# Kernel tuning notes

Measured on AMD Instinct MI355X. Metric: run time of the kernel, lower is better.

## Reference

```python
import jax, jax.numpy as jnp
import numpy as np

jax.config.update("jax_enable_x64", True)

STRIDE = 1
PADDING = 1


def _im2col(x, k, s):
    # x: (n, c, H, W) already padded. Returns (n, c*k*k, oh*ow) with
    # channel-major, then (kh, kw) ordering -- matching torch unfold/img2col.
    n, c, H, W = x.shape
    oh = (H - k) // s + 1
    ow = (W - k) // s + 1
    # k*k = 9 slices: small fixed loop over kernel offsets, fully vectorized
    # over batch/channel/spatial dims.
    patches = jnp.stack(
        [x[:, :, i:i + s * (oh - 1) + 1:s, j:j + s * (ow - 1) + 1:s]
         for i in range(k) for j in range(k)],
        axis=2,
    )  # (n, c, k*k, oh, ow)
    return patches.reshape(n, c * k * k, oh * ow)


def setup_inputs() -> dict:
    key = jax.random.key(0)
    k1, k2, k3 = jax.random.split(key, 3)
    x = jax.random.randint(k1, (32, 64, 56, 56), 0, 65536, dtype=jnp.int64)
    weight = jax.random.randint(k2, (64, 64, 3, 3), 0, 65536, dtype=jnp.int64)
    bias = jax.random.randint(k3, (64,), 0, 65536, dtype=jnp.int64)
    return {"x": x, "weight": weight, "bias": bias}


def reference(x, weight, bias):
    kN, kC, k, _ = weight.shape
    n, c, H, W = x.shape
    oh = (H - k + 2 * PADDING) // STRIDE + 1
    ow = (W - k + 2 * PADDING) // STRIDE + 1
    # pad spatial dims with zeros (ring zero)
    xp = jnp.pad(x, ((0, 0), (0, 0), (PADDING, PADDING), (PADDING, PADDING)))
    cols = _im2col(xp, k, STRIDE)              # (n, c*k*k, L)
    cols_t = cols.transpose(0, 2, 1)           # (n, L, c*k*k)
    w2 = weight.reshape(kN, kC * k * k).T      # (c*k*k, kN)
    # int64 matmul: overflow wraps (two's complement), matching ring Z_{2^64}
    out = jnp.einsum('nlk,ko->nlo', cols_t, w2) + bias  # (n, L, kN)
    return out.transpose(0, 2, 1).reshape(n, kN, oh, ow)
```

## Files before the change

kernel.cpp:

```cpp
#include <hip/hip_runtime.h>


typedef int v4i __attribute__((ext_vector_type(4)));

#define LCOL 144
#define LROW (58 * LCOL)

__device__ __align__(16) unsigned char g_wb[2 * 9 * 64 * 64];
__device__ unsigned g_off[64];

static __device__ __forceinline__ unsigned bsum(unsigned v, unsigned acc) {
#if __has_builtin(__builtin_amdgcn_sad_u8)
    return __builtin_amdgcn_sad_u8(v, 0u, acc);
#else
    return acc + (v & 0xFFu) + ((v >> 8) & 0xFFu) + ((v >> 16) & 0xFFu) + (v >> 24);
#endif
}

__global__ __launch_bounds__(256) void packw(const int* __restrict__ w,
                                             const int* __restrict__ bias) {
    int blk = blockIdx.x;
    if (blk < 144) {
        int i = blk * 256 + threadIdx.x;
        if (i >= 64 * 64 * 9) return;
        int k = i / 576;
        int r = i - k * 576;
        int c = r / 9;
        int t = r - c * 9;
        unsigned v = (unsigned)w[i];
        g_wb[((0 * 9 + t) * 64 + k) * 64 + c] = (unsigned char)((v & 255u) ^ 0x80u);
        g_wb[((1 * 9 + t) * 64 + k) * 64 + c] = (unsigned char)(((v >> 8) & 255u) ^ 0x80u);
    } else {
        int k    = threadIdx.x >> 2;
        int part = threadIdx.x & 3;
        int s0 = 0, s1 = 0;
        for (int j = part * 144; j < part * 144 + 144; ++j) {
            unsigned W = (unsigned)w[k * 576 + j];
            s0 += (int)(W & 255u);
            s1 += (int)((W >> 8) & 255u);
        }
        s0 += __shfl_xor(s0, 1); s0 += __shfl_xor(s0, 2);
        s1 += __shfl_xor(s1, 1); s1 += __shfl_xor(s1, 2);
        if (part == 0) {
            s0 -= 73728;
            s1 -= 73728;
            unsigned ws = (unsigned)(s0 + 256 * s1);
            g_off[k] = (unsigned)bias[k] + 32896u * ws + 1082146816u * 576u;
        }
    }
}

__global__ __launch_bounds__(256, 2) void secconv(const int* __restrict__ x,
                                                  int* __restrict__ out)
{
    __shared__ unsigned char sx[6 * LROW];
    __shared__ int ss[6 * 58];

    const int tid  = threadIdx.x;
    const int blk  = blockIdx.x;
    const int q    = blk >> 3;
    const int rg   = q % 14;
    const int n    = (blk & 7) + 8 * (q / 14);
    const int wid  = tid >> 6;
    const int lane = tid & 63;
    const int lm   = lane & 15;
    const int lq   = lane >> 4;
    const int kp   = wid & 1;
    const int ph   = wid >> 1;
    const int kbase = kp * 32;

    for (int it = tid; it < 348; it += 256) {
        const int pr = it / 58, pc = it - pr * 58;
        const int ih = 4 * rg - 1 + pr, iw = pc - 1;
        unsigned char* ob = sx + pr * LROW + pc * LCOL;
        int S;
        if ((unsigned)ih < 56u && (unsigned)iw < 56u) {
            const int* xp = x + (long)n * 64 * 3136 + ih * 56 + iw;
            unsigned slo = 0, shi = 0;
#pragma unroll
            for (int g = 0; g < 4; ++g) {
                unsigned lo[4], hi[4];
#pragma unroll
                for (int u = 0; u < 4; ++u) {
                    const int c = g * 16 + u * 4;
                    unsigned v0 = (unsigned)xp[(c + 0) * 3136];
                    unsigned v1 = (unsigned)xp[(c + 1) * 3136];
                    unsigned v2 = (unsigned)xp[(c + 2) * 3136];
                    unsigned v3 = (unsigned)xp[(c + 3) * 3136];
                    unsigned t01 = __builtin_amdgcn_perm(v1, v0, 0x05040100u);
                    unsigned t23 = __builtin_amdgcn_perm(v3, v2, 0x05040100u);
                    unsigned lw  = __builtin_amdgcn_perm(t23, t01, 0x06040200u);
                    unsigned hw  = __builtin_amdgcn_perm(t23, t01, 0x07050301u);
                    slo = bsum(lw, slo);
                    shi = bsum(hw, shi);
                    lo[u] = lw ^ 0x80808080u;
                    hi[u] = hw ^ 0x80808080u;
                }
                *(uint4*)(ob + g * 16)      = make_uint4(lo[0], lo[1], lo[2], lo[3]);
                *(uint4*)(ob + 64 + g * 16) = make_uint4(hi[0], hi[1], hi[2], hi[3]);
            }
            S = (int)(slo + (shi << 8)) - 2105344;
        } else {
            uint4 v = make_uint4(0x80808080u, 0x80808080u, 0x80808080u, 0x80808080u);
#pragma unroll
            for (int g = 0; g < 4; ++g) {
                *(uint4*)(ob + g * 16)      = v;
                *(uint4*)(ob + 64 + g * 16) = v;
            }
            S = -2105344;
        }
        ss[it] = S;
    }

    v4i wf[2][2][9];
#pragma unroll
    for (int kt = 0; kt < 2; ++kt)
#pragma unroll
        for (int l = 0; l < 2; ++l)
#pragma unroll
            for (int t = 0; t < 9; ++t)
                wf[kt][l][t] = *(const v4i*)(g_wb +
                    ((l * 9 + t) * 64 + (kbase + kt * 16 + lm)) * 64 + lq * 16);
    unsigned offv[2][4];
#pragma unroll
    for (int kt = 0; kt < 2; ++kt)
#pragma unroll
        for (int r = 0; r < 4; ++r)
            offv[kt][r] = g_off[kbase + kt * 16 + lq * 4 + r];

    __syncthreads();

    const int r8 = lm >> 3, c8 = lm & 7;
    const int lrow = 2 * ph + r8;
    const unsigned char* lbase = sx + lrow * LROW + c8 * LCOL + lq * 16;

    for (int t = 0; t < 7; ++t) {
        const unsigned char* tb = lbase + t * 8 * LCOL;
        v4i a00[2] = {{0,0,0,0},{0,0,0,0}}, a01[2] = {{0,0,0,0},{0,0,0,0}};
        v4i a10[2] = {{0,0,0,0},{0,0,0,0}}, a11[2] = {{0,0,0,0},{0,0,0,0}};
#pragma unroll
        for (int tap = 0; tap < 9; ++tap) {
            const int dr = tap / 3, dc = tap - (tap / 3) * 3;
            const unsigned char* pp = tb + dr * LROW + dc * LCOL;
            v4i bl = *(const v4i*)(pp);
            v4i bh = *(const v4i*)(pp + 64);
#pragma unroll
            for (int kt = 0; kt < 2; ++kt) {
                a00[kt] = __builtin_amdgcn_mfma_i32_16x16x64_i8(wf[kt][0][tap], bl, a00[kt], 0, 0, 0);
                a01[kt] = __builtin_amdgcn_mfma_i32_16x16x64_i8(wf[kt][0][tap], bh, a01[kt], 0, 0, 0);
                a10[kt] = __builtin_amdgcn_mfma_i32_16x16x64_i8(wf[kt][1][tap], bl, a10[kt], 0, 0, 0);
                a11[kt] = __builtin_amdgcn_mfma_i32_16x16x64_i8(wf[kt][1][tap], bh, a11[kt], 0, 0, 0);
            }
        }

        const int pc = t * 8 + c8;
        int Q = 0;
#pragma unroll
        for (int dr = 0; dr < 3; ++dr)
#pragma unroll
            for (int dc = 0; dc < 3; ++dc)
                Q += ss[(lrow + dr) * 58 + pc + dc];
        const unsigned qq = 32896u * (unsigned)Q;

        const long pix = (long)(4 * rg + lrow) * 56 + pc;
#pragma unroll
        for (int kt = 0; kt < 2; ++kt) {
            const long ob = ((long)n * 64 + kbase + kt * 16 + lq * 4) * 3136 + pix;
#pragma unroll
            for (int r = 0; r < 4; ++r) {
                unsigned val = (unsigned)a00[kt][r]
                             + (((unsigned)a01[kt][r] + (unsigned)a10[kt][r]) << 8)
                             + ((unsigned)a11[kt][r] << 16)
                             + qq + offv[kt][r];
                out[ob + (long)r * 3136] = (int)val;
            }
        }
    }
}

extern "C" void kernel_launch(void* const* d_in, const int* in_sizes, int n_in,
                              void* d_out, int out_size, void* d_ws, size_t ws_size,
                              hipStream_t stream)
{
    const int* x    = (const int*)d_in[0];
    const int* w    = (const int*)d_in[1];
    const int* bias = (const int*)d_in[2];
    int* out        = (int*)d_out;

    packw  <<<dim3(145), dim3(256), 0, stream>>>(w, bias);
    secconv<<<dim3(448), dim3(256), 0, stream>>>(x, out);
}
```

Baseline: 97.13 us.

## Double-buffer column chunks in LDS and remap warps to output-channel slices

The kernel no longer stages all 58 columns of the six input rows into shared memory before any compute starts. It packs 10-column chunks into a double-buffered LDS area and prepares the next chunk after each tile's MFMA work. Each wave now owns 16 output channels and covers both row pairs, so it loads half as many weight fragments while doing the same MFMA work per tile. It also raises wave priority around the MFMA loop. The cost is a barrier per tile and packing spread across all threads with shuffle reductions. The goal is lower LDS footprint, higher occupancy and overlap of global loads with matrix work.

After: 108.0 us. 1.11x slower.

```diff
diff --git a/kernel.cpp b/kernel.cpp
--- a/kernel.cpp
+++ b/kernel.cpp
@@ -4,7 +4,8 @@
 typedef int v4i __attribute__((ext_vector_type(4)));
 
 #define LCOL 144
-#define LROW (58 * LCOL)
+#define CROW (10 * LCOL)
+#define CBUF (6 * CROW)
 
 __device__ __align__(16) unsigned char g_wb[2 * 9 * 64 * 64];
 __device__ unsigned g_off[64];
@@ -50,11 +51,45 @@
     }
 }
 
+#define PACK_CHUNK(IWB, BUF) do {                                              \
+    unsigned xv[16];                                                           \
+    _Pragma("unroll")                                                          \
+    for (int i_ = 0; i_ < 16; ++i_) xv[i_] = 0u;                               \
+    const int iw_ = (IWB) + pcz;                                               \
+    if (pk && rowok && (unsigned)iw_ < 56u) {                                  \
+        const int* xp_ = x + xbase + ih * 56 + iw_;                            \
+        _Pragma("unroll")                                                      \
+        for (int i_ = 0; i_ < 16; ++i_)                                        \
+            xv[i_] = (unsigned)xp_[(g * 16 + i_) * 3136];                      \
+    }                                                                          \
+    unsigned slo_ = 0, shi_ = 0, lo_[4], hi_[4];                               \
+    _Pragma("unroll")                                                          \
+    for (int u_ = 0; u_ < 4; ++u_) {                                           \
+        unsigned t01_ = __builtin_amdgcn_perm(xv[4 * u_ + 1], xv[4 * u_ + 0], 0x05040100u); \
+        unsigned t23_ = __builtin_amdgcn_perm(xv[4 * u_ + 3], xv[4 * u_ + 2], 0x05040100u); \
+        unsigned lw_  = __builtin_amdgcn_perm(t23_, t01_, 0x06040200u);        \
+        unsigned hw_  = __builtin_amdgcn_perm(t23_, t01_, 0x07050301u);        \
+        slo_ = bsum(lw_, slo_);                                                \
+        shi_ = bsum(hw_, shi_);                                                \
+        lo_[u_] = lw_ ^ 0x80808080u;                                           \
+        hi_[u_] = hw_ ^ 0x80808080u;                                           \
+    }                                                                          \
+    int s_ = (int)(slo_ + (shi_ << 8));                                        \
+    s_ += __shfl_xor(s_, 1);                                                   \
+    s_ += __shfl_xor(s_, 2);                                                   \
+    if (pk) {                                                                  \
+        unsigned char* ob_ = sx + (BUF) * CBUF + pr * CROW + pcz * LCOL + g * 16; \
+        *(uint4*)(ob_)      = make_uint4(lo_[0], lo_[1], lo_[2], lo_[3]);      \
+        *(uint4*)(ob_ + 64) = make_uint4(hi_[0], hi_[1], hi_[2], hi_[3]);      \
+        if (g == 0) ss[BUF][pr][pcz] = s_ - 2105344;            \
+    }                                                                          \
+} while (0)
+
 __global__ __launch_bounds__(256, 2) void secconv(const int* __restrict__ x,
                                                   int* __restrict__ out)
 {
-    __shared__ unsigned char sx[6 * LROW];
-    __shared__ int ss[6 * 58];
+    __shared__ __align__(16) unsigned char sx[2 * CBUF];
+    __shared__ int ss[2][6][12];
 
     const int tid  = threadIdx.x;
     const int blk  = blockIdx.x;
@@ -65,116 +100,82 @@
     const int lane = tid & 63;
     const int lm   = lane & 15;
     const int lq   = lane >> 4;
-    const int kp   = wid & 1;
-    const int ph   = wid >> 1;
-    const int kbase = kp * 32;
+    const int r8   = lm >> 3;
+    const int c8   = lm & 7;
 
-    for (int it = tid; it < 348; it += 256) {
-        const int pr = it / 58, pc = it - pr * 58;
-        const int ih = 4 * rg - 1 + pr, iw = pc - 1;
-        unsigned char* ob = sx + pr * LROW + pc * LCOL;
-        int S;
-        if ((unsigned)ih < 56u && (unsigned)iw < 56u) {
-            const int* xp = x + (long)n * 64 * 3136 + ih * 56 + iw;
-            unsigned slo = 0, shi = 0;
+    const int  pix   = tid >> 2;
+    const int  g     = tid & 3;
+    const int  pr    = pix / 10;
+    const int  pcz   = pix - 10 * pr;
+    const bool pk    = tid < 240;
+    const int  ih    = 4 * rg - 1 + pr;
+    const bool rowok = (unsigned)ih < 56u;
+    const long xbase = (long)n * 64 * 3136;
+
+    v4i wf[2][9];
 #pragma unroll
-            for (int g = 0; g < 4; ++g) {
-                unsigned lo[4], hi[4];
+    for (int l = 0; l < 2; ++l)
 #pragma unroll
-                for (int u = 0; u < 4; ++u) {
-                    const int c = g * 16 + u * 4;
-                    unsigned v0 = (unsigned)xp[(c + 0) * 3136];
-                    unsigned v1 = (unsigned)xp[(c + 1) * 3136];
-                    unsigned v2 = (unsigned)xp[(c + 2) * 3136];
-                    unsigned v3 = (unsigned)xp[(c + 3) * 3136];
-                    unsigned t01 = __builtin_amdgcn_perm(v1, v0, 0x05040100u);
-                    unsigned t23 = __builtin_amdgcn_perm(v3, v2, 0x05040100u);
-                    unsigned lw  = __builtin_amdgcn_perm(t23, t01, 0x06040200u);
-                    unsigned hw  = __builtin_amdgcn_perm(t23, t01, 0x07050301u);
-                    slo = bsum(lw, slo);
-                    shi = bsum(hw, shi);
-                    lo[u] = lw ^ 0x80808080u;
-                    hi[u] = hw ^ 0x80808080u;
-                }
-                *(uint4*)(ob + g * 16)      = make_uint4(lo[0], lo[1], lo[2], lo[3]);
-                *(uint4*)(ob + 64 + g * 16) = make_uint4(hi[0], hi[1], hi[2], hi[3]);
-            }
-            S = (int)(slo + (shi << 8)) - 2105344;
-        } else {
-            uint4 v = make_uint4(0x80808080u, 0x80808080u, 0x80808080u, 0x80808080u);
+        for (int tp = 0; tp < 9; ++tp)
+            wf[l][tp] = *(const v4i*)(g_wb +
+                (((l * 9 + tp) * 64) + (wid * 16 + lm)) * 64 + lq * 16);
+    unsigned offv[4];
 #pragma unroll
-            for (int g = 0; g < 4; ++g) {
-                *(uint4*)(ob + g * 16)      = v;
-                *(uint4*)(ob + 64 + g * 16) = v;
-            }
-            S = -2105344;
-        }
-        ss[it] = S;
-    }
+    for (int r = 0; r < 4; ++r) offv[r] = g_off[wid * 16 + lq * 4 + r];
 
-    v4i wf[2][2][9];
-#pragma unroll
-    for (int kt = 0; kt < 2; ++kt)
-#pragma unroll
-        for (int l = 0; l < 2; ++l)
-#pragma unroll
-            for (int t = 0; t < 9; ++t)
-                wf[kt][l][t] = *(const v4i*)(g_wb +
-                    ((l * 9 + t) * 64 + (kbase + kt * 16 + lm)) * 64 + lq * 16);
-    unsigned offv[2][4];
-#pragma unroll
-    for (int kt = 0; kt < 2; ++kt)
-#pragma unroll
-        for (int r = 0; r < 4; ++r)
-            offv[kt][r] = g_off[kbase + kt * 16 + lq * 4 + r];
-
+    PACK_CHUNK(-1, 0);
     __syncthreads();
 
-    const int r8 = lm >> 3, c8 = lm & 7;
-    const int lrow = 2 * ph + r8;
-    const unsigned char* lbase = sx + lrow * LROW + c8 * LCOL + lq * 16;
+    for (int t = 0; t < 7; ++t) {
+        const int cur = t & 1;
 
-    for (int t = 0; t < 7; ++t) {
-        const unsigned char* tb = lbase + t * 8 * LCOL;
+        int cs[5];
+#pragma unroll
+        for (int j = 0; j < 5; ++j)
+            cs[j] = ss[cur][r8 + j][c8] + ss[cur][r8 + j][c8 + 1] + ss[cur][r8 + j][c8 + 2];
+        const unsigned qq0 = 32896u * (unsigned)(cs[0] + cs[1] + cs[2]);
+        const unsigned qq1 = 32896u * (unsigned)(cs[2] + cs[3] + cs[4]);
+
         v4i a00[2] = {{0,0,0,0},{0,0,0,0}}, a01[2] = {{0,0,0,0},{0,0,0,0}};
         v4i a10[2] = {{0,0,0,0},{0,0,0,0}}, a11[2] = {{0,0,0,0},{0,0,0,0}};
+        const unsigned char* cb = sx + cur * CBUF + r8 * CROW + c8 * LCOL + lq * 16;
+        __builtin_amdgcn_s_setprio(1);
 #pragma unroll
         for (int tap = 0; tap < 9; ++tap) {
-            const int dr = tap / 3, dc = tap - (tap / 3) * 3;
-            const unsigned char* pp = tb + dr * LROW + dc * LCOL;
-            v4i bl = *(const v4i*)(pp);
-            v4i bh = *(const v4i*)(pp + 64);
+            const int dr = tap / 3, dc = tap - 3 * (tap / 3);
+            const unsigned char* pb = cb + dr * CROW + dc * LCOL;
+            v4i bl0 = *(const v4i*)(pb);
+            v4i bh0 = *(const v4i*)(pb + 64);
+            v4i bl1 = *(const v4i*)(pb + 2 * CROW);
+            v4i bh1 = *(const v4i*)(pb + 2 * CROW + 64);
+            a00[0] = __builtin_amdgcn_mfma_i32_16x16x64_i8(wf[0][tap], bl0, a00[0], 0, 0, 0);
+            a01[0] = __builtin_amdgcn_mfma_i32_16x16x64_i8(wf[0][tap], bh0, a01[0], 0, 0, 0);
+            a10[0] = __builtin_amdgcn_mfma_i32_16x16x64_i8(wf[1][tap], bl0, a10[0], 0, 0, 0);
+            a11[0] = __builtin_amdgcn_mfma_i32_16x16x64_i8(wf[1][tap], bh0, a11[0], 0, 0, 0);
+            a00[1] = __builtin_amdgcn_mfma_i32_16x16x64_i8(wf[0][tap], bl1, a00[1], 0, 0, 0);
+            a01[1] = __builtin_amdgcn_mfma_i32_16x16x64_i8(wf[0][tap], bh1, a01[1], 0, 0, 0);
+            a10[1] = __builtin_amdgcn_mfma_i32_16x16x64_i8(wf[1][tap], bl1, a10[1], 0, 0, 0);
+            a11[1] = __builtin_amdgcn_mfma_i32_16x16x64_i8(wf[1][tap], bh1, a11[1], 0, 0, 0);
+        }
+        __builtin_amdgcn_s_setprio(0);
+
 #pragma unroll
-            for (int kt = 0; kt < 2; ++kt) {
-                a00[kt] = __builtin_amdgcn_mfma_i32_16x16x64_i8(wf[kt][0][tap], bl, a00[kt], 0, 0, 0);
-                a01[kt] = __builtin_amdgcn_mfma_i32_16x16x64_i8(wf[kt][0][tap], bh, a01[kt], 0, 0, 0);
-                a10[kt] = __builtin_amdgcn_mfma_i32_16x16x64_i8(wf[kt][1][tap], bl, a10[kt], 0, 0, 0);
-                a11[kt] = __builtin_amdgcn_mfma_i32_16x16x64_i8(wf[kt][1][tap], bh, a11[kt], 0, 0, 0);
+        for (int ph = 0; ph < 2; ++ph) {
+            const unsigned qq = ph ? qq1 : qq0;
+            const long ob = ((long)n * 64 + wid * 16 + lq * 4) * 3136
+                          + (long)(4 * rg + 2 * ph + r8) * 56 + 8 * t + c8;
+#pragma unroll
+            for (int r = 0; r < 4; ++r) {
+                unsigned val = (unsigned)a00[ph][r]
+                             + (((unsigned)a01[ph][r] + (unsigned)a10[ph][r]) << 8)
+                             + ((unsigned)a11[ph][r] << 16)
+                             + qq + offv[r];
+                out[ob + (long)r * 3136] = (int)val;
             }
         }
 
-        const int pc = t * 8 + c8;
-        int Q = 0;
-#pragma unroll
-        for (int dr = 0; dr < 3; ++dr)
-#pragma unroll
-            for (int dc = 0; dc < 3; ++dc)
-                Q += ss[(lrow + dr) * 58 + pc + dc];
-        const unsigned qq = 32896u * (unsigned)Q;
-
-        const long pix = (long)(4 * rg + lrow) * 56 + pc;
-#pragma unroll
-        for (int kt = 0; kt < 2; ++kt) {
-            const long ob = ((long)n * 64 + kbase + kt * 16 + lq * 4) * 3136 + pix;
-#pragma unroll
-            for (int r = 0; r < 4; ++r) {
-                unsigned val = (unsigned)a00[kt][r]
-                             + (((unsigned)a01[kt][r] + (unsigned)a10[kt][r]) << 8)
-                             + ((unsigned)a11[kt][r] << 16)
-                             + qq + offv[kt][r];
-                out[ob + (long)r * 3136] = (int)val;
-            }
-        }
+        if (t < 6) PACK_CHUNK(8 * (t + 1) - 1, cur ^ 1);
+        __syncthreads();
     }
 }
 
```

## Vectorize input staging with 16-byte loads and raise MFMA wave priority

Applied to the files above, without the earlier changes.

The shared-memory staging loop now gives each thread four adjacent pixels across sixteen channels. It reads them with 16-byte vector loads instead of one scalar load per channel per pixel. Per-pixel byte sums are combined across the four channel-group lanes with xor shuffles. The zero-padding border cells are filled by separate code. s_setprio is also raised around the MFMA tap loop so matrix work gets issue priority over the other waves. This cuts load instruction count and address arithmetic in the prologue, at the cost of more registers and shuffle-based reduction logic.

Measured after the change: 99.54 us. 2.5% more time.

```diff
diff --git a/kernel.cpp b/kernel.cpp
--- a/kernel.cpp
+++ b/kernel.cpp
@@ -69,47 +69,65 @@
     const int ph   = wid >> 1;
     const int kbase = kp * 32;
 
-    for (int it = tid; it < 348; it += 256) {
-        const int pr = it / 58, pc = it - pr * 58;
-        const int ih = 4 * rg - 1 + pr, iw = pc - 1;
-        unsigned char* ob = sx + pr * LROW + pc * LCOL;
-        int S;
-        if ((unsigned)ih < 56u && (unsigned)iw < 56u) {
-            const int* xp = x + (long)n * 64 * 3136 + ih * 56 + iw;
-            unsigned slo = 0, shi = 0;
-#pragma unroll
-            for (int g = 0; g < 4; ++g) {
-                unsigned lo[4], hi[4];
-#pragma unroll
-                for (int u = 0; u < 4; ++u) {
-                    const int c = g * 16 + u * 4;
-                    unsigned v0 = (unsigned)xp[(c + 0) * 3136];
-                    unsigned v1 = (unsigned)xp[(c + 1) * 3136];
-                    unsigned v2 = (unsigned)xp[(c + 2) * 3136];
-                    unsigned v3 = (unsigned)xp[(c + 3) * 3136];
-                    unsigned t01 = __builtin_amdgcn_perm(v1, v0, 0x05040100u);
-                    unsigned t23 = __builtin_amdgcn_perm(v3, v2, 0x05040100u);
+    const uint4 fillv = make_uint4(0x80808080u, 0x80808080u, 0x80808080u, 0x80808080u);
+    if (tid < 96) {
+        const int cell = tid >> 3, i = tid & 7;
+        const int pr = cell >> 1, pc = (cell & 1) * 57;
+        *(uint4*)(sx + pr * LROW + pc * LCOL + i * 16) = fillv;
+        if (i == 0) ss[pr * 58 + pc] = -2105344;
+    }
+    const int brow = (rg == 0) ? 0 : (rg == 13 ? 5 : -1);
+    if (brow >= 0) {
+        for (int j = tid; j < 464; j += 256) {
+            const int cell = j >> 3, i = j & 7;
+            *(uint4*)(sx + brow * LROW + cell * LCOL + i * 16) = fillv;
+            if (i == 0) ss[brow * 58 + cell] = -2105344;
+        }
+    }
+
+    const int* bp = x + (long)n * 64 * 3136;
+    for (int task = tid; task < 336; task += 256) {
+        const int pr = task / 56;
+        const int rr = task - pr * 56;
+        const int pq = rr >> 2;
+        const int c4 = rr & 3;
+        const int ih = 4 * rg - 1 + pr;
+        if ((unsigned)ih < 56u) {
+            const int voff = c4 * 16 * 3136 + ih * 56 + pq * 4;
+            unsigned slo[4] = {0, 0, 0, 0}, shi[4] = {0, 0, 0, 0};
+            unsigned lov[4][4], hiv[4][4];
+#pragma unroll
+            for (int cb = 0; cb < 4; ++cb) {
+                v4i q0 = *(const v4i*)(bp + (cb * 4 + 0) * 3136 + voff);
+                v4i q1 = *(const v4i*)(bp + (cb * 4 + 1) * 3136 + voff);
+                v4i q2 = *(const v4i*)(bp + (cb * 4 + 2) * 3136 + voff);
+                v4i q3 = *(const v4i*)(bp + (cb * 4 + 3) * 3136 + voff);
+#pragma unroll
+                for (int p = 0; p < 4; ++p) {
+                    unsigned t01 = __builtin_amdgcn_perm((unsigned)q1[p], (unsigned)q0[p], 0x05040100u);
+                    unsigned t23 = __builtin_amdgcn_perm((unsigned)q3[p], (unsigned)q2[p], 0x05040100u);
                     unsigned lw  = __builtin_amdgcn_perm(t23, t01, 0x06040200u);
                     unsigned hw  = __builtin_amdgcn_perm(t23, t01, 0x07050301u);
-                    slo = bsum(lw, slo);
-                    shi = bsum(hw, shi);
-                    lo[u] = lw ^ 0x80808080u;
-                    hi[u] = hw ^ 0x80808080u;
+                    slo[p] = bsum(lw, slo[p]);
+                    shi[p] = bsum(hw, shi[p]);
+                    lov[cb][p] = lw ^ 0x80808080u;
+                    hiv[cb][p] = hw ^ 0x80808080u;
                 }
-                *(uint4*)(ob + g * 16)      = make_uint4(lo[0], lo[1], lo[2], lo[3]);
-                *(uint4*)(ob + 64 + g * 16) = make_uint4(hi[0], hi[1], hi[2], hi[3]);
-            }
-            S = (int)(slo + (shi << 8)) - 2105344;
-        } else {
-            uint4 v = make_uint4(0x80808080u, 0x80808080u, 0x80808080u, 0x80808080u);
-#pragma unroll
-            for (int g = 0; g < 4; ++g) {
-                *(uint4*)(ob + g * 16)      = v;
-                *(uint4*)(ob + 64 + g * 16) = v;
-            }
-            S = -2105344;
-        }
-        ss[it] = S;
+            }
+            unsigned char* ob = sx + pr * LROW + (pq * 4 + 1) * LCOL + c4 * 16;
+#pragma unroll
+            for (int p = 0; p < 4; ++p) {
+                *(uint4*)(ob + p * LCOL)      = make_uint4(lov[0][p], lov[1][p], lov[2][p], lov[3][p]);
+                *(uint4*)(ob + p * LCOL + 64) = make_uint4(hiv[0][p], hiv[1][p], hiv[2][p], hiv[3][p]);
+            }
+#pragma unroll
+            for (int p = 0; p < 4; ++p) {
+                int s = (int)(slo[p] + (shi[p] << 8));
+                s += __shfl_xor(s, 1);
+                s += __shfl_xor(s, 2);
+                if (c4 == 0) ss[pr * 58 + pq * 4 + 1 + p] = s - 2105344;
+            }
+        }
     }
 
     v4i wf[2][2][9];
@@ -138,6 +156,7 @@
         const unsigned char* tb = lbase + t * 8 * LCOL;
         v4i a00[2] = {{0,0,0,0},{0,0,0,0}}, a01[2] = {{0,0,0,0},{0,0,0,0}};
         v4i a10[2] = {{0,0,0,0},{0,0,0,0}}, a11[2] = {{0,0,0,0},{0,0,0,0}};
+        __builtin_amdgcn_s_setprio(1);
 #pragma unroll
         for (int tap = 0; tap < 9; ++tap) {
             const int dr = tap / 3, dc = tap - (tap / 3) * 3;
@@ -152,6 +171,7 @@
                 a11[kt] = __builtin_amdgcn_mfma_i32_16x16x64_i8(wf[kt][1][tap], bh, a11[kt], 0, 0, 0);
             }
         }
+        __builtin_amdgcn_s_setprio(0);
 
         const int pc = t * 8 + c8;
         int Q = 0;
```
